# Kernel tuning notes

Hardware: AMD Instinct MI355X
Metric: run time of the kernel (lower is better)

Reference implementation:

```python
import jax, jax.numpy as jnp
from jax import lax
import numpy as np

K = 8          # local window radius -> (2K+1)^2 = 289 offsets
TOPK = 256     # topk channels kept for fg/bg correlation
EPS = 1e-5     # torch InstanceNorm2d default eps


def _conv3(x, w, b):
    # 3x3 conv, stride 1, pad 1, NCHW/OIHW
    y = lax.conv_general_dilated(x, w, (1, 1), ((1, 1), (1, 1)),
                                 dimension_numbers=('NCHW', 'OIHW', 'NCHW'))
    return y + b[None, :, None, None]


def _inorm(x):
    # InstanceNorm2d(affine=False): per (b,c) normalization over HxW, biased var
    m = jnp.mean(x, axis=(2, 3), keepdims=True)
    v = jnp.mean((x - m) ** 2, axis=(2, 3), keepdims=True)
    return (x - m) * lax.rsqrt(v + EPS)


def _aic(x, w1, b1, w2, b2):
    # AIC(in, hidden): conv3x3(in->hidden)+IN+ReLU -> conv3x3(hidden->in)+IN+ReLU
    h = jax.nn.relu(_inorm(_conv3(x, w1, b1)))
    return jax.nn.relu(_inorm(_conv3(h, w2, b2)))


def _amaxpool(x, H, W):
    # adaptive_max_pool2d with exact integer factor (384/48 = 8)
    kh, kw = x.shape[2] // H, x.shape[3] // W
    return lax.reduce_window(x, -jnp.inf, lax.max, (1, 1, kh, kw), (1, 1, kh, kw), 'VALID')


def _topk_c(x, k=TOPK):
    # topk over channel axis, values sorted descending (matches torch.topk)
    v, _ = lax.top_k(jnp.transpose(x, (0, 2, 3, 1)), k)  # [B,H,W,k]
    return jnp.transpose(v, (0, 3, 1, 2))                 # [B,k,H,W]


def _resize_ac(x, H, W):
    # bilinear interpolate, align_corners=True
    B, C, h, w = x.shape
    def grid(n_out, n_in):
        if n_out == 1:
            return jnp.zeros((1,), jnp.float32)
        return jnp.arange(n_out, dtype=jnp.float32) * ((n_in - 1) / (n_out - 1))
    ys, xs = grid(H, h), grid(W, w)
    y0 = jnp.clip(jnp.floor(ys).astype(jnp.int32), 0, h - 1)
    y1 = jnp.minimum(y0 + 1, h - 1)
    x0 = jnp.clip(jnp.floor(xs).astype(jnp.int32), 0, w - 1)
    x1 = jnp.minimum(x0 + 1, w - 1)
    wy = (ys - y0.astype(jnp.float32))[None, None, :, None]
    wx = (xs - x0.astype(jnp.float32))[None, None, None, :]
    rows = x[:, :, y0, :] * (1.0 - wy) + x[:, :, y1, :] * wy  # [B,C,H,w]
    return rows[:, :, :, x0] * (1.0 - wx) + rows[:, :, :, x1] * wx


def _forward(p3, p2, p1, kg1, klp, key_mask, pre_mask,
             conv_top_w, conv_top_b,
             aic_top_w1, aic_top_b1, aic_top_w2, aic_top_b2,
             r1a_w1, r1a_b1, r1a_w2, r1a_b2,
             r1b_w1, r1b_b1, r1b_w2, r1b_b2,
             r2a_w1, r2a_b1, r2a_w2, r2a_b2,
             r2b_w1, r2b_b1, r2b_w2, r2b_b2,
             dec_conv1_w, dec_conv1_b, pred_w, pred_b):
    B, _, H, W = kg1.shape  # kg1: [B, H*W, H, W]
    # --- Global, mode=2: fg/bg topk over the global correlation volume ---
    gm = _amaxpool(key_mask, H, W).reshape(B, H * W, 1, 1)
    gf = _topk_c(kg1 * gm)
    gb = _topk_c(kg1 * (1.0 - gm))
    # --- Local, mode=2: unfold mask into 17x17 windows, fg/bg topk ---
    lm = _amaxpool(pre_mask, H, W)                       # [B,1,H,W]
    lmp = jnp.pad(lm, ((0, 0), (0, 0), (K, K), (K, K)))  # zero pad (FF.pad default)
    patches = lax.conv_general_dilated_patches(
        lmp, (2 * K + 1, 2 * K + 1), (1, 1), 'VALID',
        dimension_numbers=('NCHW', 'OIHW', 'NCHW'))      # [B,289,H,W], ch = dy*17+dx
    lf = _topk_c(klp * patches)
    lb = _topk_c(klp * (1.0 - patches))
    # --- fuse at p3 resolution ---
    pm = _amaxpool(pre_mask, H, W)
    x = jnp.concatenate([p3, gf, gb, lf, lb, pm], axis=1)  # [B, 256*5+1, H, W]
    x = _conv3(x, conv_top_w, conv_top_b)                  # 1281 -> 256
    x = _aic(x, aic_top_w1, aic_top_b1, aic_top_w2, aic_top_b2)
    # --- Decoder: Refine(256,64) -> conv 256->64 -> Refine(64,64) -> pred ---
    y = _resize_ac(x, p2.shape[2], p2.shape[3])
    y = _aic(y, r1a_w1, r1a_b1, r1a_w2, r1a_b2)
    y = y + p2
    y = _aic(y, r1b_w1, r1b_b1, r1b_w2, r1b_b2)
    y = _conv3(y, dec_conv1_w, dec_conv1_b)
    z = _resize_ac(y, p1.shape[2], p1.shape[3])
    z = _aic(z, r2a_w1, r2a_b1, r2a_w2, r2a_b2)
    z = z + p1
    z = _aic(z, r2b_w1, r2b_b1, r2b_w2, r2b_b2)
    return jax.nn.sigmoid(_conv3(z, pred_w, pred_b))       # [B,1,192,192]


def setup_inputs() -> dict:
    key = jax.random.key(0)
    ks = jax.random.split(key, 40)
    B, H, W = 2, 48, 48
    inp = {}
    inp['p3'] = jax.random.normal(ks[0], (B, 256, H, W), jnp.float32)
    inp['p2'] = jax.random.normal(ks[1], (B, 256, 2 * H, 2 * W), jnp.float32)
    inp['p1'] = jax.random.normal(ks[2], (B, 64, 4 * H, 4 * W), jnp.float32)
    inp['kg1'] = jax.random.normal(ks[3], (B, H * W, H, W), jnp.float32)
    inp['klp'] = jax.random.normal(ks[4], (B, (2 * K + 1) ** 2, H, W), jnp.float32)
    inp['key_mask'] = jax.random.uniform(ks[5], (B, 1, 8 * H, 8 * W), dtype=jnp.float32)
    inp['pre_mask'] = jax.random.uniform(ks[6], (B, 1, 8 * H, 8 * W), dtype=jnp.float32)
    i = [7]
    def p(shape, s=0.05):
        w = jax.random.normal(ks[i[0]], shape, jnp.float32) * s
        i[0] += 1
        return w
    inp['conv_top_w'] = p((256, 256 * 5 + 1, 3, 3))
    inp['conv_top_b'] = jnp.zeros((256,), jnp.float32)
    for nm, (ci, ch) in [('aic_top', (256, 64)), ('r1a', (256, 64)), ('r1b', (256, 64)),
                         ('r2a', (64, 64)), ('r2b', (64, 64))]:
        inp[nm + '_w1'] = p((ch, ci, 3, 3)); inp[nm + '_b1'] = jnp.zeros((ch,), jnp.float32)
        inp[nm + '_w2'] = p((ci, ch, 3, 3)); inp[nm + '_b2'] = jnp.zeros((ci,), jnp.float32)
    inp['dec_conv1_w'] = p((64, 256, 3, 3)); inp['dec_conv1_b'] = jnp.zeros((64,), jnp.float32)
    inp['pred_w'] = p((1, 64, 3, 3)); inp['pred_b'] = jnp.zeros((1,), jnp.float32)
    return inp


def reference(p3, p2, p1, kg1, klp, key_mask, pre_mask,
              conv_top_w, conv_top_b,
              aic_top_w1, aic_top_b1, aic_top_w2, aic_top_b2,
              r1a_w1, r1a_b1, r1a_w2, r1a_b2,
              r1b_w1, r1b_b1, r1b_w2, r1b_b2,
              r2a_w1, r2a_b1, r2a_w2, r2a_b2,
              r2b_w1, r2b_b1, r2b_w2, r2b_b2,
              dec_conv1_w, dec_conv1_b, pred_w, pred_b):
    return _forward(p3, p2, p1, kg1, klp, key_mask, pre_mask,
                    conv_top_w, conv_top_b,
                    aic_top_w1, aic_top_b1, aic_top_w2, aic_top_b2,
                    r1a_w1, r1a_b1, r1a_w2, r1a_b2,
                    r1b_w1, r1b_b1, r1b_w2, r1b_b2,
                    r2a_w1, r2a_b1, r2a_w2, r2a_b2,
                    r2b_w1, r2b_b1, r2b_w2, r2b_b2,
                    dec_conv1_w, dec_conv1_b, pred_w, pred_b)
```

## Files before the change

### kernel.cpp

```cpp
#include <hip/hip_runtime.h>
#include <math.h>

#define TPB 256

typedef _Float16 h8 __attribute__((ext_vector_type(8)));
typedef float f4 __attribute__((ext_vector_type(4)));
typedef unsigned short ushort_t;

__device__ __forceinline__ unsigned short f2bf(float x) {
  unsigned int u = __float_as_uint(x);
  unsigned int r = (u + 0x7fffu + ((u >> 16) & 1u)) >> 16;
  return (unsigned short)r;
}
__device__ __forceinline__ float bf2f(unsigned short h) {
  return __uint_as_float(((unsigned int)h) << 16);
}
__device__ __forceinline__ ushort_t f2h(float x) {
  _Float16 h = (_Float16)x;
  return *(ushort_t*)&h;
}
__device__ __forceinline__ float h2f(ushort_t u) {
  _Float16 h = *(_Float16*)&u;
  return (float)h;
}
__device__ __forceinline__ unsigned key16_of(float x) {
  unsigned h = (unsigned)f2h(x);
  return h ^ ((h >> 15) ? 0xFFFFu : 0x8000u);
}
__device__ __forceinline__ ushort_t un_key16(unsigned k) {
  return (ushort_t)(k ^ ((k & 0x8000u) ? 0x8000u : 0xFFFFu));
}

__global__ __launch_bounds__(TPB) void pool8_kernel(const float* __restrict__ in,
                                                    float* __restrict__ out, int total) {
  int idx = blockIdx.x * TPB + threadIdx.x;
  if (idx >= total) return;
  int b = idx / 2304, yx = idx - b * 2304;
  int y = yx / 48, x = yx - y * 48;
  const float* p = in + ((size_t)b * 384 + (size_t)y * 8) * 384 + (size_t)x * 8;
  float m = -INFINITY;
#pragma unroll
  for (int i = 0; i < 8; ++i)
#pragma unroll
    for (int j = 0; j < 8; ++j) m = fmaxf(m, p[(size_t)i * 384 + j]);
  out[idx] = m;
}

__global__ __launch_bounds__(TPB) void tposef_kernel(const float* __restrict__ src,
                                                     float* __restrict__ dst, int C, int HW,
                                                     int DS) {
  __shared__ float tile[64][65];
  int px0 = blockIdx.x * 64;
  int c0 = blockIdx.y * 64;
  int b = blockIdx.z;
  int tid = threadIdx.x;
#pragma unroll
  for (int i = 0; i < 16; ++i) {
    int c = (tid >> 6) + i * 4, p = tid & 63;
    tile[c][p] = src[((size_t)b * C + c0 + c) * HW + px0 + p];
  }
  __syncthreads();
#pragma unroll
  for (int i = 0; i < 16; ++i) {
    int c = tid & 63, p = (tid >> 6) + i * 4;
    dst[((size_t)b * HW + px0 + p) * DS + c0 + c] = tile[c][p];
  }
}

__global__ __launch_bounds__(TPB) void tposeg_kernel(const float* __restrict__ src,
                                                     float* __restrict__ dst, int C, int HW,
                                                     int DS) {
  __shared__ float tile[64][65];
  int px0 = blockIdx.x * 64;
  int c0 = blockIdx.y * 64;
  int b = blockIdx.z;
  int tid = threadIdx.x;
#pragma unroll
  for (int i = 0; i < 16; ++i) {
    int c = (tid >> 6) + i * 4, p = tid & 63;
    float v = 0.f;
    if (c0 + c < C) v = src[((size_t)b * C + c0 + c) * HW + px0 + p];
    tile[c][p] = v;
  }
  __syncthreads();
#pragma unroll
  for (int i = 0; i < 16; ++i) {
    int c = tid & 63, p = (tid >> 6) + i * 4;
    if (c0 + c < C)
      dst[((size_t)b * HW + px0 + p) * DS + c0 + c] = tile[c][p];
  }
}

__global__ __launch_bounds__(TPB) void tposeh_kernel(const float* __restrict__ src,
                                                     ushort_t* __restrict__ dst, int C, int HW,
                                                     int DS) {
  __shared__ float tile[64][65];
  int px0 = blockIdx.x * 64;
  int c0 = blockIdx.y * 64;
  int b = blockIdx.z;
  int tid = threadIdx.x;
#pragma unroll
  for (int i = 0; i < 16; ++i) {
    int c = (tid >> 6) + i * 4, p = tid & 63;
    tile[c][p] = src[((size_t)b * C + c0 + c) * HW + px0 + p];
  }
  __syncthreads();
#pragma unroll
  for (int i = 0; i < 16; ++i) {
    int c = tid & 63, p = (tid >> 6) + i * 4;
    dst[((size_t)b * HW + px0 + p) * DS + c0 + c] = f2h(tile[c][p]);
  }
}

__global__ __launch_bounds__(TPB) void topk_global_kernel(const float* __restrict__ kgT,
                                                          const float* __restrict__ gm,
                                                          ushort_t* __restrict__ xcat) {
  __shared__ unsigned histF[4][256], histB[4][256];
  __shared__ ushort_t soutF[256], soutB[256];
  __shared__ unsigned selT[2], selA[2];
  __shared__ unsigned cntG[2], cntE[2];
  const int tid = threadIdx.x;
  const int lane = tid & 63, wid = tid >> 6;
  int bid = blockIdx.x;
  int b = bid / 2304, yx = bid - b * 2304;
  const float* kp = kgT + ((size_t)b * 2304 + yx) * 2304;
  const float* gp = gm + (size_t)b * 2304;
  unsigned kF[9], kB[9];
#pragma unroll
  for (int j = 0; j < 9; ++j) {
    int i = tid + 256 * j;
    float v = kp[i];
    float g = gp[i];
    kF[j] = key16_of(v * g);
    kB[j] = key16_of(v * (1.0f - g));
  }
#pragma unroll
  for (int w = 0; w < 4; ++w) {
    histF[w][tid] = 0;
    histB[w][tid] = 0;
  }
  __syncthreads();
#pragma unroll
  for (int j = 0; j < 9; ++j) {
    atomicAdd(&histF[wid][kF[j] >> 8], 1u);
    atomicAdd(&histB[wid][kB[j] >> 8], 1u);
  }
  __syncthreads();
  if (wid < 2) {
    unsigned(*hh)[256] = wid ? histB : histF;
    unsigned h0 = hh[0][4 * lane] + hh[1][4 * lane] + hh[2][4 * lane] + hh[3][4 * lane];
    unsigned h1 = hh[0][4 * lane + 1] + hh[1][4 * lane + 1] + hh[2][4 * lane + 1] +
                  hh[3][4 * lane + 1];
    unsigned h2 = hh[0][4 * lane + 2] + hh[1][4 * lane + 2] + hh[2][4 * lane + 2] +
                  hh[3][4 * lane + 2];
    unsigned h3 = hh[0][4 * lane + 3] + hh[1][4 * lane + 3] + hh[2][4 * lane + 3] +
                  hh[3][4 * lane + 3];
    unsigned x = h0 + h1 + h2 + h3;
#pragma unroll
    for (int d = 1; d < 64; d <<= 1) {
      unsigned y = __shfl_down(x, d, 64);
      if (lane + d < 64) x += y;
    }
    unsigned long long m = __ballot(x >= 256u);
    int tl = 63 - __clzll(m);
    if (lane == tl) {
      unsigned s1 = x - h0, s2 = s1 - h1, s3 = s2 - h2, s4 = s3 - h3;
      int jj;
      unsigned A;
      if (s3 >= 256u) { jj = 3; A = s4; }
      else if (s2 >= 256u) { jj = 2; A = s3; }
      else if (s1 >= 256u) { jj = 1; A = s2; }
      else { jj = 0; A = s1; }
      selT[wid] = 4 * tl + jj;
      selA[wid] = A;
    }
  }
  __syncthreads();
  const unsigned T0F = selT[0], gt0F = selA[0];
  const unsigned T0B = selT[1], gt0B = selA[1];
  const unsigned KF = 256u - gt0F, KB = 256u - gt0B;
  histF[0][tid] = 0;
  histB[0][tid] = 0;
  __syncthreads();
#pragma unroll
  for (int j = 0; j < 9; ++j) {
    if ((kF[j] >> 8) == T0F) atomicAdd(&histF[0][kF[j] & 0xFFu], 1u);
    if ((kB[j] >> 8) == T0B) atomicAdd(&histB[0][kB[j] & 0xFFu], 1u);
  }
  __syncthreads();
  if (wid < 2) {
    unsigned* h = wid ? histB[0] : histF[0];
    unsigned K = wid ? KB : KF;
    unsigned h0 = h[4 * lane], h1 = h[4 * lane + 1];
    unsigned h2 = h[4 * lane + 2], h3 = h[4 * lane + 3];
    unsigned x = h0 + h1 + h2 + h3;
#pragma unroll
    for (int d = 1; d < 64; d <<= 1) {
      unsigned y = __shfl_down(x, d, 64);
      if (lane + d < 64) x += y;
    }
    unsigned long long m = __ballot(x >= K);
    int tl = 63 - __clzll(m);
    if (lane == tl) {
      unsigned s1 = x - h0, s2 = s1 - h1, s3 = s2 - h2, s4 = s3 - h3;
      int jj;
      unsigned A;
      if (s3 >= K) { jj = 3; A = s4; }
      else if (s2 >= K) { jj = 2; A = s3; }
      else if (s1 >= K) { jj = 1; A = s2; }
      else { jj = 0; A = s1; }
      selT[wid] = 4 * tl + jj;
      selA[wid] = A;
    }
  }
  __syncthreads();
  const unsigned tF = (T0F << 8) | selT[0];
  const unsigned tB = (T0B << 8) | selT[1];
  const unsigned nGTF = gt0F + selA[0], needF = 256u - nGTF;
  const unsigned nGTB = gt0B + selA[1], needB = 256u - nGTB;
  if (tid == 0) { cntG[0] = 0; cntG[1] = 0; cntE[0] = 0; cntE[1] = 0; }
  __syncthreads();
#pragma unroll
  for (int j = 0; j < 9; ++j) {
    unsigned k = kF[j];
    if (k > tF) soutF[atomicAdd(&cntG[0], 1u)] = (ushort_t)k;
    else if (k == tF) {
      unsigned e = atomicAdd(&cntE[0], 1u);
      if (e < needF) soutF[nGTF + e] = (ushort_t)tF;
    }
    k = kB[j];
    if (k > tB) soutB[atomicAdd(&cntG[1], 1u)] = (ushort_t)k;
    else if (k == tB) {
      unsigned e = atomicAdd(&cntE[1], 1u);
      if (e < needB) soutB[nGTB + e] = (ushort_t)tB;
    }
  }
  __syncthreads();
  if (wid < 2) {
    ushort_t* sarr = wid ? soutB : soutF;
    for (int kk = 2; kk <= 256; kk <<= 1) {
      for (int j = kk >> 1; j > 0; j >>= 1) {
#pragma unroll
        for (int r = 0; r < 2; ++r) {
          int p = lane + r * 64;
          int t = (p & (j - 1)) | ((p & ~(j - 1)) << 1);
          int ixj = t | j;
          bool up = ((t & kk) == 0);
          ushort_t a = sarr[t], c = sarr[ixj];
          if (up ? (a > c) : (a < c)) { sarr[t] = c; sarr[ixj] = a; }
        }
        __builtin_amdgcn_wave_barrier();
      }
    }
  }
  __syncthreads();
  size_t base = ((size_t)(b * 2304 + yx)) * 1312;
  xcat[base + 256 + tid] = un_key16((unsigned)soutF[255 - tid]);
  xcat[base + 512 + tid] = un_key16((unsigned)soutB[255 - tid]);
}

__global__ __launch_bounds__(64) void topk_local_kernel(const float* __restrict__ klpT,
                                                        const float* __restrict__ lm,
                                                        ushort_t* __restrict__ xcat) {
  __shared__ float sf[512];
  __shared__ float sb[512];
  const int lane = threadIdx.x;
  const int pix = blockIdx.x;
  const int b = pix / 2304;
  const int yx = pix - b * 2304;
  const int y = yx / 48, x = yx - y * 48;
  const float* kp = klpT + (size_t)pix * 320;
#pragma unroll
  for (int r = 0; r < 8; ++r) {
    int i = lane + r * 64;
    float vf = -INFINITY, vb = -INFINITY;
    if (i < 289) {
      int dy = i / 17, dx = i - dy * 17;
      int sy = y + dy - 8, sx = x + dx - 8;
      float pv = 0.f;
      if (sy >= 0 && sy < 48 && sx >= 0 && sx < 48) pv = lm[(size_t)b * 2304 + sy * 48 + sx];
      float v = kp[i];
      vf = v * pv;
      vb = v * (1.0f - pv);
    }
    sf[i] = vf;
    sb[i] = vb;
  }
  __builtin_amdgcn_wave_barrier();
  for (int k = 2; k <= 512; k <<= 1) {
    for (int j = k >> 1; j > 0; j >>= 1) {
#pragma unroll
      for (int r = 0; r < 4; ++r) {
        int p = lane + r * 64;
        int t = (p & (j - 1)) | ((p & ~(j - 1)) << 1);
        int ixj = t | j;
        bool up = ((t & k) == 0);
        float a = sf[t], c = sf[ixj];
        if (up ? (a > c) : (a < c)) { sf[t] = c; sf[ixj] = a; }
        a = sb[t]; c = sb[ixj];
        if (up ? (a > c) : (a < c)) { sb[t] = c; sb[ixj] = a; }
      }
      __builtin_amdgcn_wave_barrier();
    }
  }
  size_t base = (size_t)pix * 1312;
#pragma unroll
  for (int r = 0; r < 4; ++r) {
    int t = lane + r * 64;
    xcat[base + 768 + t] = f2h(sf[511 - t]);
    xcat[base + 1024 + t] = f2h(sb[511 - t]);
  }
}

__global__ __launch_bounds__(TPB) void pm_pad_kernel(const float* __restrict__ lm,
                                                     ushort_t* __restrict__ xcat) {
  int idx = blockIdx.x * TPB + threadIdx.x;
  if (idx >= 2 * 2304 * 32) return;
  int ch = idx & 31;
  int r = idx >> 5;
  xcat[(size_t)r * 1312 + 1280 + ch] = (ch == 0) ? f2h(lm[r]) : (ushort_t)0;
}

struct WallDesc {
  const float* src[13];
  int CinW[13], CIP[13], CoutPad[13], CoutReal[13];
  unsigned start[14];
  int n;
};
__global__ __launch_bounds__(TPB) void wconv_all_kernel(WallDesc D, ushort_t* __restrict__ whi,
                                                        int total) {
  int i = blockIdx.x * TPB + threadIdx.x;
  if (i >= total) return;
  int k = 0;
  while (k + 1 < D.n && (unsigned)i >= D.start[k + 1]) ++k;
  int j = i - D.start[k];
  int e = j & 7;
  int t = j >> 3;
  int l16 = t & 15; t >>= 4;
  int h4 = t & 3; t >>= 2;
  int NCOG = D.CoutPad[k] >> 4;
  int cog = t % NCOG; t /= NCOG;
  int kykx = t % 9;
  int chunk = t / 9;
  int co = cog * 16 + l16;
  int ci = chunk * 32 + h4 * 8 + e;
  float v = 0.f;
  if (ci < D.CinW[k] && co < D.CoutReal[k])
    v = D.src[k][((size_t)co * D.CinW[k] + ci) * 9 + kykx];
  whi[i] = f2h(v);
}

template <int NORM>
__device__ __forceinline__ uint4 norm8(uint4 v, const float* __restrict__ nmean,
                                       const float* __restrict__ ninv,
                                       const void* __restrict__ nres, size_t mb,
                                       size_t pxoff) {
  float f[8];
  f[0] = h2f((ushort_t)(v.x & 0xffff)); f[1] = h2f((ushort_t)(v.x >> 16));
  f[2] = h2f((ushort_t)(v.y & 0xffff)); f[3] = h2f((ushort_t)(v.y >> 16));
  f[4] = h2f((ushort_t)(v.z & 0xffff)); f[5] = h2f((ushort_t)(v.z >> 16));
  f[6] = h2f((ushort_t)(v.w & 0xffff)); f[7] = h2f((ushort_t)(v.w >> 16));
  float4 m0 = *(const float4*)(nmean + mb);
  float4 m1 = *(const float4*)(nmean + mb + 4);
  float4 i0 = *(const float4*)(ninv + mb);
  float4 i1 = *(const float4*)(ninv + mb + 4);
  float o[8];
  o[0] = fmaxf((f[0] - m0.x) * i0.x, 0.f);
  o[1] = fmaxf((f[1] - m0.y) * i0.y, 0.f);
  o[2] = fmaxf((f[2] - m0.z) * i0.z, 0.f);
  o[3] = fmaxf((f[3] - m0.w) * i0.w, 0.f);
  o[4] = fmaxf((f[4] - m1.x) * i1.x, 0.f);
  o[5] = fmaxf((f[5] - m1.y) * i1.y, 0.f);
  o[6] = fmaxf((f[6] - m1.z) * i1.z, 0.f);
  o[7] = fmaxf((f[7] - m1.w) * i1.w, 0.f);
  if (NORM == 2) {
    uint4 rv = *(const uint4*)((const ushort_t*)nres + pxoff);
    o[0] += h2f((ushort_t)(rv.x & 0xffff)); o[1] += h2f((ushort_t)(rv.x >> 16));
    o[2] += h2f((ushort_t)(rv.y & 0xffff)); o[3] += h2f((ushort_t)(rv.y >> 16));
    o[4] += h2f((ushort_t)(rv.z & 0xffff)); o[5] += h2f((ushort_t)(rv.z >> 16));
    o[6] += h2f((ushort_t)(rv.w & 0xffff)); o[7] += h2f((ushort_t)(rv.w >> 16));
  } else if (NORM == 3) {
    const float* rp = (const float*)nres + pxoff;
    float4 r0 = *(const float4*)rp;
    float4 r1 = *(const float4*)(rp + 4);
    o[0] += r0.x; o[1] += r0.y; o[2] += r0.z; o[3] += r0.w;
    o[4] += r1.x; o[5] += r1.y; o[6] += r1.z; o[7] += r1.w;
  }
  uint4 out;
  out.x = (unsigned)f2h(o[0]) | ((unsigned)f2h(o[1]) << 16);
  out.y = (unsigned)f2h(o[2]) | ((unsigned)f2h(o[3]) << 16);
  out.z = (unsigned)f2h(o[4]) | ((unsigned)f2h(o[5]) << 16);
  out.w = (unsigned)f2h(o[6]) | ((unsigned)f2h(o[7]) << 16);
  return out;
}

template <int MFR, int ACT, int STAT, int GEOM, int NORM>
__global__ __launch_bounds__(TPB) void conv_mfma_kernel(
    const ushort_t* __restrict__ in, const ushort_t* __restrict__ whi,
    const float* __restrict__ bias,
    ushort_t* __restrict__ outh, float* __restrict__ outf, ushort_t* __restrict__ partial,
    float* __restrict__ stat, int ntiles,
    const float* __restrict__ nmean, const float* __restrict__ ninv,
    const void* __restrict__ nres,
    int hin, int win, float rs,
    int CIP, int Cout, int H, int W, int S, int ci_per_s) {
  const int NPIX = (GEOM == 1) ? 100 : 180;
  const int PITCH = 10;
  __shared__ uint4 sB[(GEOM == 1) ? 800 : 1440];
  const int MB = (GEOM == 1) ? 64 : MFR * 32;
  const int tid = threadIdx.x;
  const int lane = tid & 63;
  const int lo16 = lane & 15, hi4 = lane >> 4;
  const int wid = tid >> 6;
  const int wco = (GEOM == 1) ? wid : (wid & 1);
  const int wpx = (GEOM == 1) ? 0 : (wid >> 1);
  const int tilesX = W >> 3;
  const int tx0 = (blockIdx.x % tilesX) << 3;
  const int ty0 = (blockIdx.x / tilesX) << ((GEOM == 1) ? 3 : 4);
  const int s = blockIdx.y % S;
  const int co0 = (blockIdx.y / S) * MB;
  const int b = blockIdx.z;
  const int NCOG = Cout >> 4;
  const size_t HW = (size_t)H * W;
  const ushort_t* inb = in + (size_t)b * HW * CIP;
  const ushort_t* srcb = in + (size_t)b * hin * win * CIP;
  int ci_begin = s * ci_per_s;
  int ci_end = ci_begin + ci_per_s;
  if (ci_end > CIP) ci_end = CIP;
  f4 acc[MFR][4];
#pragma unroll
  for (int m = 0; m < MFR; ++m)
#pragma unroll
    for (int n = 0; n < 4; ++n) acc[m][n] = (f4){0.f, 0.f, 0.f, 0.f};

  for (int ci0 = ci_begin; ci0 < ci_end; ci0 += 64) {
    const bool has2 = (ci0 + 32 < ci_end);
    __syncthreads();
#pragma unroll
    for (int it = 0; it < 6; ++it) {
      int u = it * TPB + tid;
      if (u < NPIX * 8) {
        int q4 = u / NPIX;
        int pix = u - q4 * NPIX;
        int prow = pix / PITCH, pcol = pix - prow * PITCH;
        int gy = ty0 - 1 + prow, gx = tx0 - 1 + pcol;
        int ci = ci0 + q4 * 8;
        bool inbp = (ci < CIP && gy >= 0 && gy < H && gx >= 0 && gx < W);
        uint4 v = {0u, 0u, 0u, 0u};
        if (inbp) {
          if (NORM <= 3) {
            v = *(const uint4*)(inb + ((size_t)gy * W + gx) * CIP + ci);
            if (NORM != 0) {
              size_t mb = (size_t)b * CIP + ci;
              size_t pxoff = ((size_t)b * HW + (size_t)gy * W + gx) * CIP + ci;
              v = norm8<NORM>(v, nmean, ninv, nres, mb, pxoff);
            }
          } else {
            float ys = gy * rs, xs = gx * rs;
            int y0 = (int)floorf(ys);
            if (y0 > hin - 1) y0 = hin - 1;
            int x0 = (int)floorf(xs);
            if (x0 > win - 1) x0 = win - 1;
            int y1 = y0 + 1 < hin ? y0 + 1 : hin - 1;
            int x1 = x0 + 1 < win ? x0 + 1 : win - 1;
            float wy = ys - (float)y0, wx = xs - (float)x0;
            uint4 s00 = *(const uint4*)(srcb + ((size_t)y0 * win + x0) * CIP + ci);
            uint4 s01 = *(const uint4*)(srcb + ((size_t)y0 * win + x1) * CIP + ci);
            uint4 s10 = *(const uint4*)(srcb + ((size_t)y1 * win + x0) * CIP + ci);
            uint4 s11 = *(const uint4*)(srcb + ((size_t)y1 * win + x1) * CIP + ci);
            float w00 = (1.f - wy) * (1.f - wx), w01 = (1.f - wy) * wx;
            float w10 = wy * (1.f - wx), w11 = wy * wx;
            union U8 { uint4 q; ushort_t sv[8]; };
            U8 u00, u01, u10, u11, uo;
            u00.q = s00; u01.q = s01; u10.q = s10; u11.q = s11;
#pragma unroll
            for (int k8 = 0; k8 < 8; ++k8) {
              float val = h2f(u00.sv[k8]) * w00 + h2f(u01.sv[k8]) * w01 +
                          h2f(u10.sv[k8]) * w10 + h2f(u11.sv[k8]) * w11;
              uo.sv[k8] = f2h(val);
            }
            v = uo.q;
          }
        }
        sB[q4 * NPIX + pix] = v;
      }
    }
    __syncthreads();
#pragma unroll
    for (int h = 0; h < 2; ++h) {
      if (h == 1 && !has2) continue;
      const int chunkIdx = (ci0 >> 5) + h;
#pragma unroll
      for (int ky = 0; ky < 3; ++ky) {
#pragma unroll
        for (int kx = 0; kx < 3; ++kx) {
          const int kykx = ky * 3 + kx;
          h8 ah[MFR];
#pragma unroll
          for (int m = 0; m < MFR; ++m) {
            int cog = (co0 + wco * (GEOM == 1 ? 16 : (MB / 2)) + m * 16) >> 4;
            size_t woff = (((size_t)chunkIdx * 9 + kykx) * NCOG + cog) * 512 + (size_t)lane * 8;
            ah[m] = *(const h8*)(whi + woff);
          }
          h8 bf[4];
#pragma unroll
          for (int n = 0; n < 4; ++n) {
            int pix = (wpx * 8 + n * 2 + (lo16 >> 3) + ky) * PITCH + (lo16 & 7) + kx;
            union { uint4 q; h8 v; } ub;
            ub.q = sB[(h * 4 + hi4) * NPIX + pix];
            bf[n] = ub.v;
          }
#pragma unroll
          for (int m = 0; m < MFR; ++m)
#pragma unroll
            for (int n = 0; n < 4; ++n)
              acc[m][n] = __builtin_amdgcn_mfma_f32_16x16x32_f16(ah[m], bf[n], acc[m][n], 0, 0, 0);
        }
      }
    }
  }

#pragma unroll
  for (int m = 0; m < MFR; ++m) {
#pragma unroll
    for (int n = 0; n < 4; ++n) {
      int py = ty0 + wpx * 8 + n * 2 + (lo16 >> 3);
      int pxx = tx0 + (lo16 & 7);
      int co_r0 = co0 + wco * (GEOM == 1 ? 16 : (MB / 2)) + m * 16 + hi4 * 4;
      if (ACT == 1) {
        if (wco == 0 && m == 0 && hi4 == 0) {
          float v = acc[0][n][0] + bias[0];
          outf[(size_t)b * HW + (size_t)py * W + pxx] = 1.0f / (1.0f + expf(-v));
        }
      } else if (S == 1) {
        float4 bv = *(const float4*)(bias + co_r0);
        unsigned w0 = (unsigned)f2h(acc[m][n][0] + bv.x) |
                      ((unsigned)f2h(acc[m][n][1] + bv.y) << 16);
        unsigned w1 = (unsigned)f2h(acc[m][n][2] + bv.z) |
                      ((unsigned)f2h(acc[m][n][3] + bv.w) << 16);
        uint2 o = {w0, w1};
        *(uint2*)(outh + (((size_t)b * HW + (size_t)py * W + pxx) * Cout + co_r0)) = o;
        if (STAT) {
          acc[m][n][0] = h2f((ushort_t)(w0 & 0xffff));
          acc[m][n][1] = h2f((ushort_t)(w0 >> 16));
          acc[m][n][2] = h2f((ushort_t)(w1 & 0xffff));
          acc[m][n][3] = h2f((ushort_t)(w1 >> 16));
        }
      } else {
        uint2 o;
        o.x = (unsigned)f2h(acc[m][n][0]) | ((unsigned)f2h(acc[m][n][1]) << 16);
        o.y = (unsigned)f2h(acc[m][n][2]) | ((unsigned)f2h(acc[m][n][3]) << 16);
        *(uint2*)(partial + (((size_t)(s * 2 + b) * HW + (size_t)py * W + pxx) * Cout + co_r0)) = o;
      }
    }
  }

  if (STAT) {
    __syncthreads();
    f4* lredS = (f4*)sB;
    f4* lredQ = lredS + 32;
    if (GEOM == 1) {
      f4 sv = acc[0][0] + acc[0][1] + acc[0][2] + acc[0][3];
      f4 qv = acc[0][0] * acc[0][0] + acc[0][1] * acc[0][1] + acc[0][2] * acc[0][2] +
              acc[0][3] * acc[0][3];
#pragma unroll
      for (int off = 1; off < 16; off <<= 1) {
#pragma unroll
        for (int kq = 0; kq < 4; ++kq) {
          sv[kq] += __shfl_xor(sv[kq], off, 64);
          qv[kq] += __shfl_xor(qv[kq], off, 64);
        }
      }
      if (lo16 == 0) {
        lredS[wid * 4 + hi4] = sv;
        lredQ[wid * 4 + hi4] = qv;
      }
      __syncthreads();
      if (tid < 16) {
        int widT = tid >> 2, h4T = tid & 3;
        int c = co0 + widT * 16 + h4T * 4;
        size_t sbase = ((size_t)b * ntiles + blockIdx.x) * (size_t)(Cout * 2);
        *(f4*)(stat + sbase + c) = lredS[tid];
        *(f4*)(stat + sbase + Cout + c) = lredQ[tid];
      }
    } else {
#pragma unroll
      for (int m = 0; m < MFR; ++m) {
        f4 sv = acc[m][0] + acc[m][1] + acc[m][2] + acc[m][3];
        f4 qv = acc[m][0] * acc[m][0] + acc[m][1] * acc[m][1] + acc[m][2] * acc[m][2] +
                acc[m][3] * acc[m][3];
#pragma unroll
        for (int off = 1; off < 16; off <<= 1) {
#pragma unroll
          for (int kq = 0; kq < 4; ++kq) {
            sv[kq] += __shfl_xor(sv[kq], off, 64);
            qv[kq] += __shfl_xor(qv[kq], off, 64);
          }
        }
        if (lo16 == 0) {
          lredS[(wid * MFR + m) * 4 + hi4] = sv;
          lredQ[(wid * MFR + m) * 4 + hi4] = qv;
        }
      }
      __syncthreads();
      if (tid < 2 * MFR * 4) {
        int wcoT = tid / (MFR * 4);
        int r = tid % (MFR * 4);
        int mT = r / 4;
        int h4T = r % 4;
        f4 sv = lredS[((wcoT)*MFR + mT) * 4 + h4T] + lredS[((wcoT + 2) * MFR + mT) * 4 + h4T];
        f4 qv = lredQ[((wcoT)*MFR + mT) * 4 + h4T] + lredQ[((wcoT + 2) * MFR + mT) * 4 + h4T];
        int c = co0 + wcoT * (MB / 2) + mT * 16 + h4T * 4;
        size_t sbase = ((size_t)b * ntiles + blockIdx.x) * (size_t)(Cout * 2);
        *(f4*)(stat + sbase + c) = sv;
        *(f4*)(stat + sbase + Cout + c) = qv;
      }
    }
  }
}

__global__ __launch_bounds__(TPB) void pred_kernel(const ushort_t* __restrict__ in,
                                                   const float* __restrict__ w,
                                                   const float* __restrict__ bias,
                                                   const float* __restrict__ nmean,
                                                   const float* __restrict__ ninv,
                                                   float* __restrict__ outp) {
  __shared__ uint4 hal[324 * 9];
  __shared__ float wl[576];
  const int tid = threadIdx.x;
  const int tx0 = (blockIdx.x % 12) * 16;
  const int ty0 = (blockIdx.x / 12) * 16;
  const int b = blockIdx.y;
  const ushort_t* inb = in + (size_t)b * 36864 * 64;
  for (int u = tid; u < 576; u += TPB) {
    int ci = u & 63, kk = u >> 6;
    wl[u] = w[(size_t)ci * 9 + kk];
  }
  for (int u = tid; u < 2592; u += TPB) {
    int px = u >> 3, q4 = u & 7;
    int r = px / 18, c = px - r * 18;
    int gy = ty0 - 1 + r, gx = tx0 - 1 + c;
    uint4 v = {0u, 0u, 0u, 0u};
    if (gy >= 0 && gy < 192 && gx >= 0 && gx < 192) {
      v = *(const uint4*)(inb + ((size_t)gy * 192 + gx) * 64 + q4 * 8);
      v = norm8<1>(v, nmean, ninv, nullptr, (size_t)b * 64 + q4 * 8, 0);
    }
    hal[px * 9 + q4] = v;
  }
  __syncthreads();
  const int ty = tid >> 4, tx = tid & 15;
  float acc = bias[0];
#pragma unroll
  for (int ky = 0; ky < 3; ++ky) {
#pragma unroll
    for (int kx = 0; kx < 3; ++kx) {
      int base = ((ty + ky) * 18 + tx + kx) * 9;
      const float* wp = &wl[(ky * 3 + kx) * 64];
#pragma unroll
      for (int q = 0; q < 8; ++q) {
        uint4 v = hal[base + q];
        const float* w8 = wp + q * 8;
        acc = fmaf(h2f((ushort_t)(v.x & 0xffff)), w8[0], acc);
        acc = fmaf(h2f((ushort_t)(v.x >> 16)), w8[1], acc);
        acc = fmaf(h2f((ushort_t)(v.y & 0xffff)), w8[2], acc);
        acc = fmaf(h2f((ushort_t)(v.y >> 16)), w8[3], acc);
        acc = fmaf(h2f((ushort_t)(v.z & 0xffff)), w8[4], acc);
        acc = fmaf(h2f((ushort_t)(v.z >> 16)), w8[5], acc);
        acc = fmaf(h2f((ushort_t)(v.w & 0xffff)), w8[6], acc);
        acc = fmaf(h2f((ushort_t)(v.w >> 16)), w8[7], acc);
      }
    }
  }
  outp[(size_t)b * 36864 + (size_t)(ty0 + ty) * 192 + (tx0 + tx)] =
      1.0f / (1.0f + expf(-acc));
}

template <int STAT>
__global__ __launch_bounds__(TPB) void reduce_nhwc_kernel(const ushort_t* __restrict__ partial,
                                                          const float* __restrict__ bias,
                                                          ushort_t* __restrict__ outh,
                                                          float* __restrict__ stat, int bpb,
                                                          int S, int Cout, int HW, int total4) {
  int i = blockIdx.x * TPB + threadIdx.x;
  float4 accv = {0.f, 0.f, 0.f, 0.f};
  unsigned w0 = 0, w1 = 0;
  int e = i * 4;
  int CHW = Cout * HW;
  if (i < total4) {
    int b = e / CHW;
    int rem = e - b * CHW;
    int co = e % Cout;
    for (int ss = 0; ss < S; ++ss) {
      const uint2 t2 = *(const uint2*)(partial + (size_t)(ss * 2 + b) * CHW + rem);
      accv.x += h2f((ushort_t)(t2.x & 0xffff));
      accv.y += h2f((ushort_t)(t2.x >> 16));
      accv.z += h2f((ushort_t)(t2.y & 0xffff));
      accv.w += h2f((ushort_t)(t2.y >> 16));
    }
    float4 bv = *(const float4*)(bias + co);
    w0 = (unsigned)f2h(accv.x + bv.x) | ((unsigned)f2h(accv.y + bv.y) << 16);
    w1 = (unsigned)f2h(accv.z + bv.z) | ((unsigned)f2h(accv.w + bv.w) << 16);
    uint2 o = {w0, w1};
    *(uint2*)(outh + (size_t)b * CHW + rem) = o;
  }
  if (STAT) {
    __shared__ f4 ls[4][16], lq[4][16];
    const int tid = threadIdx.x;
    const int lane = tid & 63, wv = tid >> 6;
    f4 r;
    r[0] = h2f((ushort_t)(w0 & 0xffff));
    r[1] = h2f((ushort_t)(w0 >> 16));
    r[2] = h2f((ushort_t)(w1 & 0xffff));
    r[3] = h2f((ushort_t)(w1 >> 16));
    f4 sv = r;
    f4 qv = r * r;
#pragma unroll
    for (int kq = 0; kq < 4; ++kq) {
      sv[kq] += __shfl_down(sv[kq], 16, 64);
      qv[kq] += __shfl_down(qv[kq], 16, 64);
      sv[kq] += __shfl_down(sv[kq], 32, 64);
      qv[kq] += __shfl_down(qv[kq], 32, 64);
    }
    if (lane < 16) {
      ls[wv][lane] = sv;
      lq[wv][lane] = qv;
    }
    __syncthreads();
    if (tid < 16) {
      f4 S4 = ls[0][tid] + ls[1][tid] + ls[2][tid] + ls[3][tid];
      f4 Q4 = lq[0][tid] + lq[1][tid] + lq[2][tid] + lq[3][tid];
      int b = (blockIdx.x * (TPB * 4)) / CHW;
      int tblk = blockIdx.x - b * bpb;
      int c = tid * 4;
      size_t sbase = ((size_t)b * bpb + tblk) * (size_t)(Cout * 2);
      *(f4*)(stat + sbase + c) = S4;
      *(f4*)(stat + sbase + Cout + c) = Q4;
    }
  }
}

__global__ __launch_bounds__(TPB) void in_stats_kernel(const ushort_t* __restrict__ x,
                                                       float* __restrict__ stat, int N, int C) {
  __shared__ float ls[4][64], lq[4][64];
  int CG = C >> 6;
  int b = blockIdx.x / CG, cg = blockIdx.x % CG;
  int slice = blockIdx.y;
  int c = threadIdx.x & 63, p = threadIdx.x >> 6;
  int cnt = N >> 6;
  int base = slice * cnt;
  float s = 0.f, q = 0.f;
  const ushort_t* xp = x + ((size_t)b * N) * C + cg * 64 + c;
  for (int px = base + p; px < base + cnt; px += 4) {
    float v = h2f(xp[(size_t)px * C]);
    s += v;
    q = fmaf(v, v, q);
  }
  ls[p][c] = s;
  lq[p][c] = q;
  __syncthreads();
  if (threadIdx.x < 64) {
    float S = ls[0][threadIdx.x] + ls[1][threadIdx.x] + ls[2][threadIdx.x] + ls[3][threadIdx.x];
    float Q = lq[0][threadIdx.x] + lq[1][threadIdx.x] + lq[2][threadIdx.x] + lq[3][threadIdx.x];
    int Ctot = 2 * C;
    int idx = b * C + cg * 64 + threadIdx.x;
    stat[(size_t)(slice * Ctot + idx) * 2] = S;
    stat[(size_t)(slice * Ctot + idx) * 2 + 1] = Q;
  }
}

__global__ __launch_bounds__(TPB) void in_final_kernel(const float* __restrict__ stat,
                                                       float* __restrict__ mean,
                                                       float* __restrict__ inv, int N, int Ctot) {
  int idx = blockIdx.x * TPB + threadIdx.x;
  if (idx >= Ctot) return;
  float S = 0.f, Q = 0.f;
  for (int sl = 0; sl < 64; ++sl) {
    S += stat[(size_t)(sl * Ctot + idx) * 2];
    Q += stat[(size_t)(sl * Ctot + idx) * 2 + 1];
  }
  float m = S / (float)N;
  float var = Q / (float)N - m * m;
  if (var < 0.f) var = 0.f;
  mean[idx] = m;
  inv[idx] = 1.0f / sqrtf(var + 1e-5f);
}

__global__ __launch_bounds__(TPB) void in_final_tiles_kernel(const float* __restrict__ stat,
                                                             float* __restrict__ mean,
                                                             float* __restrict__ inv, int N,
                                                             int C, int ntiles) {
  __shared__ float rs_[TPB], rq_[TPB];
  int idx = blockIdx.x;
  int b = idx / C, c = idx % C;
  float S = 0.f, Q = 0.f;
  for (int t = threadIdx.x; t < ntiles; t += TPB) {
    size_t base = ((size_t)b * ntiles + t) * (size_t)(C * 2);
    S += stat[base + c];
    Q += stat[base + C + c];
  }
  rs_[threadIdx.x] = S;
  rq_[threadIdx.x] = Q;
  __syncthreads();
  for (int off = TPB / 2; off > 0; off >>= 1) {
    if (threadIdx.x < off) {
      rs_[threadIdx.x] += rs_[threadIdx.x + off];
      rq_[threadIdx.x] += rq_[threadIdx.x + off];
    }
    __syncthreads();
  }
  if (threadIdx.x == 0) {
    float ma = rs_[0] / (float)N;
    float var = rq_[0] / (float)N - ma * ma;
    if (var < 0.f) var = 0.f;
    mean[idx] = ma;
    inv[idx] = 1.0f / sqrtf(var + 1e-5f);
  }
}

template <int NORM>
__global__ __launch_bounds__(TPB) void resize4_kernel(const ushort_t* __restrict__ in,
                                                      ushort_t* __restrict__ out,
                                                      const float* __restrict__ nmean,
                                                      const float* __restrict__ ninv, int C,
                                                      int hin, int win, int Hout, int Wout,
                                                      float r, int total4) {
  for (int i = blockIdx.x * TPB + threadIdx.x; i < total4; i += gridDim.x * TPB) {
    int e = i * 4;
    int c = e % C;
    int t = e / C;
    int X = t % Wout;
    int t2 = t / Wout;
    int Y = t2 % Hout;
    int b = t2 / Hout;
    float ys = Y * r, xs = X * r;
    int y0 = (int)floorf(ys);
    if (y0 > hin - 1) y0 = hin - 1;
    int x0 = (int)floorf(xs);
    if (x0 > win - 1) x0 = win - 1;
    int y1 = y0 + 1 < hin ? y0 + 1 : hin - 1;
    int x1 = x0 + 1 < win ? x0 + 1 : win - 1;
    float wy = ys - (float)y0, wx = xs - (float)x0;
    const ushort_t* ip = in + ((size_t)b * hin * win) * C + c;
    uint2 a2 = *(const uint2*)(ip + ((size_t)y0 * win + x0) * C);
    uint2 b2 = *(const uint2*)(ip + ((size_t)y0 * win + x1) * C);
    uint2 c2 = *(const uint2*)(ip + ((size_t)y1 * win + x0) * C);
    uint2 d2 = *(const uint2*)(ip + ((size_t)y1 * win + x1) * C);
    float av[4], bv[4], cv[4], dv[4];
    av[0] = h2f((ushort_t)(a2.x & 0xffff)); av[1] = h2f((ushort_t)(a2.x >> 16));
    av[2] = h2f((ushort_t)(a2.y & 0xffff)); av[3] = h2f((ushort_t)(a2.y >> 16));
    bv[0] = h2f((ushort_t)(b2.x & 0xffff)); bv[1] = h2f((ushort_t)(b2.x >> 16));
    bv[2] = h2f((ushort_t)(b2.y & 0xffff)); bv[3] = h2f((ushort_t)(b2.y >> 16));
    cv[0] = h2f((ushort_t)(c2.x & 0xffff)); cv[1] = h2f((ushort_t)(c2.x >> 16));
    cv[2] = h2f((ushort_t)(c2.y & 0xffff)); cv[3] = h2f((ushort_t)(c2.y >> 16));
    dv[0] = h2f((ushort_t)(d2.x & 0xffff)); dv[1] = h2f((ushort_t)(d2.x >> 16));
    dv[2] = h2f((ushort_t)(d2.y & 0xffff)); dv[3] = h2f((ushort_t)(d2.y >> 16));
    if (NORM) {
      float4 m4 = *(const float4*)(nmean + (size_t)b * C + c);
      float4 i4 = *(const float4*)(ninv + (size_t)b * C + c);
      float mm[4] = {m4.x, m4.y, m4.z, m4.w};
      float ii[4] = {i4.x, i4.y, i4.z, i4.w};
#pragma unroll
      for (int k = 0; k < 4; ++k) {
        av[k] = fmaxf((av[k] - mm[k]) * ii[k], 0.f);
        bv[k] = fmaxf((bv[k] - mm[k]) * ii[k], 0.f);
        cv[k] = fmaxf((cv[k] - mm[k]) * ii[k], 0.f);
        dv[k] = fmaxf((dv[k] - mm[k]) * ii[k], 0.f);
      }
    }
    float w00 = (1.f - wy) * (1.f - wx), w01 = (1.f - wy) * wx;
    float w10 = wy * (1.f - wx), w11 = wy * wx;
    float o[4];
#pragma unroll
    for (int k = 0; k < 4; ++k)
      o[k] = av[k] * w00 + bv[k] * w01 + cv[k] * w10 + dv[k] * w11;
    uint2 ov;
    ov.x = (unsigned)f2h(o[0]) | ((unsigned)f2h(o[1]) << 16);
    ov.y = (unsigned)f2h(o[2]) | ((unsigned)f2h(o[3]) << 16);
    *(uint2*)(out + e) = ov;
  }
}

extern "C" void kernel_launch(void* const* d_in, const int* in_sizes, int n_in,
                              void* d_out, int out_size, void* d_ws, size_t ws_size,
                              hipStream_t stream) {
  (void)in_sizes; (void)n_in; (void)out_size;
  const float* p3 = (const float*)d_in[0];
  const float* p2 = (const float*)d_in[1];
  const float* p1 = (const float*)d_in[2];
  const float* kg1 = (const float*)d_in[3];
  const float* klp = (const float*)d_in[4];
  const float* key_mask = (const float*)d_in[5];
  const float* pre_mask = (const float*)d_in[6];
  const float* conv_top_w = (const float*)d_in[7];
  const float* conv_top_b = (const float*)d_in[8];
  const float* aic_top_w1 = (const float*)d_in[9];
  const float* aic_top_b1 = (const float*)d_in[10];
  const float* aic_top_w2 = (const float*)d_in[11];
  const float* aic_top_b2 = (const float*)d_in[12];
  const float* r1a_w1 = (const float*)d_in[13];
  const float* r1a_b1 = (const float*)d_in[14];
  const float* r1a_w2 = (const float*)d_in[15];
  const float* r1a_b2 = (const float*)d_in[16];
  const float* r1b_w1 = (const float*)d_in[17];
  const float* r1b_b1 = (const float*)d_in[18];
  const float* r1b_w2 = (const float*)d_in[19];
  const float* r1b_b2 = (const float*)d_in[20];
  const float* r2a_w1 = (const float*)d_in[21];
  const float* r2a_b1 = (const float*)d_in[22];
  const float* r2a_w2 = (const float*)d_in[23];
  const float* r2a_b2 = (const float*)d_in[24];
  const float* r2b_w1 = (const float*)d_in[25];
  const float* r2b_b1 = (const float*)d_in[26];
  const float* r2b_w2 = (const float*)d_in[27];
  const float* r2b_b2 = (const float*)d_in[28];
  const float* dec_w = (const float*)d_in[29];
  const float* dec_b = (const float*)d_in[30];
  const float* pred_w = (const float*)d_in[31];
  const float* pred_b = (const float*)d_in[32];
  float* outp = (float*)d_out;

  const size_t OFF_GM = 0;
  const size_t OFF_LM = 4608;
  const size_t OFF_STAT = 9216;
  const size_t OFF_MEAN = 304128;
  const size_t OFF_INV = 304640;
  const size_t OFF_WB = 305152;
  const size_t OFF_AH0 = 4544512;
  const size_t OFF_AH1 = 7567360;
  const size_t OFF_AH2 = 8157184;
  const size_t OFF_AH3 = 8304640;
  const size_t OFF_AH4 = 8894464;
  const size_t OFF_AH5 = 11253760;
  const size_t OFF_P1T = 13613056;
  const size_t OFF_P2T = 18331648;
  const size_t TOTAL_F = 19511296;
  if (ws_size < TOTAL_F * sizeof(float)) return;

  float* ws = (float*)d_ws;
  float* gm = ws + OFF_GM;
  float* lm = ws + OFF_LM;
  float* statb = ws + OFF_STAT;
  float* meanb = ws + OFF_MEAN;
  float* invb = ws + OFF_INV;
  ushort_t* wbh = (ushort_t*)(ws + OFF_WB);
  ushort_t* xcat_h = (ushort_t*)(ws + OFF_AH0);
  ushort_t* y96_h = (ushort_t*)(ws + OFF_AH0);
  ushort_t* a0_h = (ushort_t*)(ws + OFF_AH1);
  ushort_t* h96_h = (ushort_t*)(ws + OFF_AH1);
  ushort_t* d96_h = (ushort_t*)(ws + OFF_AH1);
  ushort_t* h48_h = (ushort_t*)(ws + OFF_AH2);
  ushort_t* a1_h = (ushort_t*)(ws + OFF_AH3);
  ushort_t* R1_h = (ushort_t*)(ws + OFF_AH4);
  ushort_t* zA_h = (ushort_t*)(ws + OFF_AH4);
  ushort_t* R0_h = (ushort_t*)(ws + OFF_AH5);
  ushort_t* zB_h = (ushort_t*)(ws + OFF_AH5);
  ushort_t* Pbuf16 = (ushort_t*)(ws + OFF_P1T);
  ushort_t* PbufTop16 = (ushort_t*)(ws + OFF_AH4);
  float* p1t = ws + OFF_P1T;
  ushort_t* p2t = (ushort_t*)(ws + OFF_P2T);
  float* kgT = ws + OFF_AH4;
  float* klpT = ws + OFF_P1T;

  WallDesc D;
  const float* wsrc[13] = {conv_top_w, aic_top_w1, aic_top_w2, r1a_w1, r1a_w2, r1b_w1,
                           r1b_w2, dec_w, r2a_w1, r2a_w2, r2b_w1, r2b_w2, pred_w};
  const int wcin[13] = {1281, 256, 64, 256, 64, 256, 64, 256, 64, 64, 64, 64, 64};
  const int wcip[13] = {1312, 256, 64, 256, 64, 256, 64, 256, 64, 64, 64, 64, 64};
  const int wcop[13] = {256, 64, 256, 64, 256, 64, 256, 64, 64, 64, 64, 64, 64};
  const int wcor[13] = {256, 64, 256, 64, 256, 64, 256, 64, 64, 64, 64, 64, 1};
  unsigned cum = 0;
  unsigned woff[13];
  for (int k = 0; k < 13; ++k) {
    D.src[k] = wsrc[k];
    D.CinW[k] = wcin[k];
    D.CIP[k] = wcip[k];
    D.CoutPad[k] = wcop[k];
    D.CoutReal[k] = wcor[k];
    D.start[k] = cum;
    woff[k] = cum;
    cum += (unsigned)(wcop[k] * 9 * wcip[k]);
  }
  D.start[13] = cum;
  D.n = 13;
  wconv_all_kernel<<<(cum + TPB - 1) / TPB, TPB, 0, stream>>>(D, wbh, (int)cum);

  pool8_kernel<<<(2 * 2304 + TPB - 1) / TPB, TPB, 0, stream>>>(key_mask, gm, 2 * 2304);
  pool8_kernel<<<(2 * 2304 + TPB - 1) / TPB, TPB, 0, stream>>>(pre_mask, lm, 2 * 2304);
  tposeg_kernel<<<dim3(36, 5, 2), TPB, 0, stream>>>(klp, klpT, 289, 2304, 320);
  topk_local_kernel<<<4608, 64, 0, stream>>>(klpT, lm, xcat_h);
  tposef_kernel<<<dim3(36, 36, 2), TPB, 0, stream>>>(kg1, kgT, 2304, 2304, 2304);
  topk_global_kernel<<<2 * 2304, TPB, 0, stream>>>(kgT, gm, xcat_h);
  tposeh_kernel<<<dim3(36, 4, 2), TPB, 0, stream>>>(p3, xcat_h, 256, 2304, 1312);
  pm_pad_kernel<<<(2 * 2304 * 32 + TPB - 1) / TPB, TPB, 0, stream>>>(lm, xcat_h);

  auto conv = [&](const ushort_t* src, int wk, const float* bb, ushort_t* dsth,
                  ushort_t* part, int CIP, int CoutPad, int H, int W, int S, int MB,
                  int geom, int redStat, int normMode, const void* res, int hin, int win,
                  float rsc) {
    const ushort_t* whiK = wbh + woff[wk];
    int chunks = CIP / 32;
    int cps = ((chunks + S - 1) / S) * 32;
    if (geom == 1) {
      int ntiles = (W / 8) * (H / 8);
      dim3 grid(ntiles, CoutPad / 64, 2);
      if (normMode == 1)
        conv_mfma_kernel<1, 0, 1, 1, 1><<<grid, TPB, 0, stream>>>(
            src, whiK, bb, dsth, nullptr, nullptr, statb, ntiles, meanb, invb, res,
            hin, win, rsc, CIP, CoutPad, H, W, 1, cps);
      else if (normMode == 3)
        conv_mfma_kernel<1, 0, 1, 1, 3><<<grid, TPB, 0, stream>>>(
            src, whiK, bb, dsth, nullptr, nullptr, statb, ntiles, meanb, invb, res,
            hin, win, rsc, CIP, CoutPad, H, W, 1, cps);
      else if (normMode == 5)
        conv_mfma_kernel<1, 0, 1, 1, 5><<<grid, TPB, 0, stream>>>(
            src, whiK, bb, dsth, nullptr, nullptr, statb, ntiles, meanb, invb, res,
            hin, win, rsc, CIP, CoutPad, H, W, 1, cps);
      else
        conv_mfma_kernel<1, 0, 1, 1, 0><<<grid, TPB, 0, stream>>>(
            src, whiK, bb, dsth, nullptr, nullptr, statb, ntiles, meanb, invb, res,
            hin, win, rsc, CIP, CoutPad, H, W, 1, cps);
      return;
    }
    int ntiles = (W / 8) * (H / 16);
    dim3 grid(ntiles, (CoutPad / MB) * S, 2);
    if (MB == 128)
      conv_mfma_kernel<4, 0, 0, 0, 0><<<grid, TPB, 0, stream>>>(
          src, whiK, bb, dsth, nullptr, part, nullptr, 0, meanb, invb, res, hin, win,
          rsc, CIP, CoutPad, H, W, S, cps);
    else if (normMode == 1)
      conv_mfma_kernel<2, 0, 0, 0, 1><<<grid, TPB, 0, stream>>>(
          src, whiK, bb, dsth, nullptr, part, nullptr, 0, meanb, invb, res, hin, win,
          rsc, CIP, CoutPad, H, W, S, cps);
    else if (normMode == 2)
      conv_mfma_kernel<2, 0, 0, 0, 2><<<grid, TPB, 0, stream>>>(
          src, whiK, bb, dsth, nullptr, part, nullptr, 0, meanb, invb, res, hin, win,
          rsc, CIP, CoutPad, H, W, S, cps);
    else
      conv_mfma_kernel<2, 0, 0, 0, 0><<<grid, TPB, 0, stream>>>(
          src, whiK, bb, dsth, nullptr, part, nullptr, 0, meanb, invb, res, hin, win,
          rsc, CIP, CoutPad, H, W, S, cps);
    if (S > 1) {
      int HW = H * W;
      int total4 = 2 * CoutPad * HW / 4;
      int nblk = (total4 + TPB - 1) / TPB;
      int bpb = (CoutPad * HW) / (TPB * 4);
      if (redStat)
        reduce_nhwc_kernel<1><<<nblk, TPB, 0, stream>>>(part, bb, dsth, statb, bpb, S,
                                                        CoutPad, HW, total4);
      else
        reduce_nhwc_kernel<0><<<nblk, TPB, 0, stream>>>(part, bb, dsth, nullptr, 0, S,
                                                        CoutPad, HW, total4);
    }
  };
  auto stats_plain = [&](ushort_t* x, int C, int N) {
    dim3 g1(2 * (C / 64), 64);
    in_stats_kernel<<<g1, TPB, 0, stream>>>(x, statb, N, C);
    int Ctot = 2 * C;
    in_final_kernel<<<(Ctot + TPB - 1) / TPB, TPB, 0, stream>>>(statb, meanb, invb, N, Ctot);
  };
  auto stats_tiles = [&](int C, int N, int ntiles) {
    in_final_tiles_kernel<<<2 * C, TPB, 0, stream>>>(statb, meanb, invb, N, C, ntiles);
  };

  conv(xcat_h, 0, conv_top_b, a0_h, PbufTop16, 1312, 256, 48, 48, 7, 128, 0, 0, 0, nullptr,
       48, 48, 1.f);
  conv(a0_h, 1, aic_top_b1, h48_h, Pbuf16, 256, 64, 48, 48, 8, 64, 0, 1, 0, nullptr, 48, 48,
       1.f);
  stats_tiles(64, 2304, 144);
  conv(h48_h, 2, aic_top_b2, a1_h, Pbuf16, 64, 256, 48, 48, 2, 64, 0, 0, 1, nullptr, 48, 48,
       1.f);
  stats_plain(a1_h, 256, 2304);

  {
    int total4 = 2 * 96 * 96 * 256 / 4;
    int g = (total4 + TPB - 1) / TPB; if (g > 4096) g = 4096;
    resize4_kernel<1><<<g, TPB, 0, stream>>>(a1_h, y96_h, meanb, invb, 256, 48, 48, 96, 96,
                                             47.f / 95.f, total4);
  }
  conv(y96_h, 3, r1a_b1, h96_h, Pbuf16, 256, 64, 96, 96, 4, 64, 0, 1, 0, nullptr, 96, 96,
       1.f);
  tposeh_kernel<<<dim3(144, 4, 2), TPB, 0, stream>>>(p2, p2t, 256, 9216, 256);
  stats_tiles(64, 9216, 576);
  conv(h96_h, 4, r1a_b2, R1_h, nullptr, 64, 256, 96, 96, 1, 64, 1, 0, 1, nullptr, 96, 96,
       1.f);
  stats_tiles(256, 9216, 144);
  conv(R1_h, 5, r1b_b1, h96_h, Pbuf16, 256, 64, 96, 96, 4, 64, 0, 1, 2, p2t, 96, 96, 1.f);
  stats_tiles(64, 9216, 576);
  conv(h96_h, 6, r1b_b2, R0_h, nullptr, 64, 256, 96, 96, 1, 64, 1, 0, 1, nullptr, 96, 96,
       1.f);
  stats_tiles(256, 9216, 144);
  conv(R0_h, 7, dec_b, d96_h, Pbuf16, 256, 64, 96, 96, 4, 64, 0, 0, 1, nullptr, 96, 96,
       1.f);
  tposef_kernel<<<dim3(576, 1, 2), TPB, 0, stream>>>(p1, p1t, 64, 36864, 64);

  conv(d96_h, 8, r2a_b1, zA_h, nullptr, 64, 64, 192, 192, 1, 64, 1, 0, 5, nullptr, 96, 96,
       95.f / 191.f);
  stats_tiles(64, 36864, 576);
  conv(zA_h, 9, r2a_b2, zB_h, nullptr, 64, 64, 192, 192, 1, 64, 1, 0, 1, nullptr, 192, 192,
       1.f);
  stats_tiles(64, 36864, 576);
  conv(zB_h, 10, r2b_b1, zA_h, nullptr, 64, 64, 192, 192, 1, 64, 1, 0, 3, p1t, 192, 192,
       1.f);
  stats_tiles(64, 36864, 576);
  conv(zA_h, 11, r2b_b2, zB_h, nullptr, 64, 64, 192, 192, 1, 64, 1, 0, 1, nullptr, 192, 192,
       1.f);
  stats_tiles(64, 36864, 576);

  pred_kernel<<<dim3(144, 2), TPB, 0, stream>>>(zB_h, pred_w, pred_b, meanb, invb, outp);
}
```

Before: 517.6 us.

## Run local top-k bitonic sort in registers with wave shuffles

The local-window top-k bitonic sort now keeps its 512 values in per-lane registers (8 per lane) instead of LDS. Compare-exchange steps with stride of 64 or more happen between registers inside a lane, and smaller strides use cross-lane xor shuffles. Four pixels are packed into each 256-thread block instead of one 64-thread block per pixel. This removes LDS traffic and wave barriers from a small kernel, at the cost of more shuffle instructions and register use.

New measurement: 514.3 us. No clear change (-0.6%).

```diff
diff --git a/kernel.cpp b/kernel.cpp
--- a/kernel.cpp
+++ b/kernel.cpp
@@ -259,20 +259,20 @@
   xcat[base + 512 + tid] = un_key16((unsigned)soutB[255 - tid]);
 }
 
-__global__ __launch_bounds__(64) void topk_local_kernel(const float* __restrict__ klpT,
-                                                        const float* __restrict__ lm,
-                                                        ushort_t* __restrict__ xcat) {
-  __shared__ float sf[512];
-  __shared__ float sb[512];
-  const int lane = threadIdx.x;
-  const int pix = blockIdx.x;
+__global__ __launch_bounds__(TPB) void topk_local_kernel(const float* __restrict__ klpT,
+                                                         const float* __restrict__ lm,
+                                                         ushort_t* __restrict__ xcat) {
+  const int lane = threadIdx.x & 63;
+  const int wid = threadIdx.x >> 6;
+  const int pix = blockIdx.x * 4 + wid;
   const int b = pix / 2304;
   const int yx = pix - b * 2304;
   const int y = yx / 48, x = yx - y * 48;
   const float* kp = klpT + (size_t)pix * 320;
+  float vF[8], vB[8];
 #pragma unroll
   for (int r = 0; r < 8; ++r) {
-    int i = lane + r * 64;
+    int i = r * 64 + lane;
     float vf = -INFINITY, vb = -INFINITY;
     if (i < 289) {
       int dy = i / 17, dx = i - dy * 17;
@@ -283,32 +283,49 @@
       vf = v * pv;
       vb = v * (1.0f - pv);
     }
-    sf[i] = vf;
-    sb[i] = vb;
-  }
-  __builtin_amdgcn_wave_barrier();
+    vF[r] = vf;
+    vB[r] = vb;
+  }
   for (int k = 2; k <= 512; k <<= 1) {
     for (int j = k >> 1; j > 0; j >>= 1) {
-#pragma unroll
-      for (int r = 0; r < 4; ++r) {
-        int p = lane + r * 64;
-        int t = (p & (j - 1)) | ((p & ~(j - 1)) << 1);
-        int ixj = t | j;
-        bool up = ((t & k) == 0);
-        float a = sf[t], c = sf[ixj];
-        if (up ? (a > c) : (a < c)) { sf[t] = c; sf[ixj] = a; }
-        a = sb[t]; c = sb[ixj];
-        if (up ? (a > c) : (a < c)) { sb[t] = c; sb[ixj] = a; }
+      if (j >= 64) {
+        const int jr = j >> 6;
+#pragma unroll
+        for (int r = 0; r < 8; ++r) {
+          if ((r & jr) == 0) {
+            const int rp = r | jr;
+            bool up = (((unsigned)(r * 64) & (unsigned)k) == 0);
+            float aF = vF[r], cF = vF[rp];
+            float aB = vB[r], cB = vB[rp];
+            if (up) {
+              vF[r] = fminf(aF, cF); vF[rp] = fmaxf(aF, cF);
+              vB[r] = fminf(aB, cB); vB[rp] = fmaxf(aB, cB);
+            } else {
+              vF[r] = fmaxf(aF, cF); vF[rp] = fminf(aF, cF);
+              vB[r] = fmaxf(aB, cB); vB[rp] = fminf(aB, cB);
+            }
+          }
+        }
+      } else {
+        bool lower = ((lane & j) == 0);
+#pragma unroll
+        for (int r = 0; r < 8; ++r) {
+          float pF = __shfl_xor(vF[r], j, 64);
+          float pB = __shfl_xor(vB[r], j, 64);
+          bool up = (((unsigned)(r * 64 + lane) & (unsigned)k) == 0);
+          bool takeMin = (lower == up);
+          vF[r] = takeMin ? fminf(vF[r], pF) : fmaxf(vF[r], pF);
+          vB[r] = takeMin ? fminf(vB[r], pB) : fmaxf(vB[r], pB);
+        }
       }
-      __builtin_amdgcn_wave_barrier();
     }
   }
   size_t base = (size_t)pix * 1312;
 #pragma unroll
-  for (int r = 0; r < 4; ++r) {
-    int t = lane + r * 64;
-    xcat[base + 768 + t] = f2h(sf[511 - t]);
-    xcat[base + 1024 + t] = f2h(sb[511 - t]);
+  for (int r = 4; r < 8; ++r) {
+    int t = 511 - (r * 64 + lane);
+    xcat[base + 768 + t] = f2h(vF[r]);
+    xcat[base + 1024 + t] = f2h(vB[r]);
   }
 }
 
@@ -987,7 +1004,7 @@
   pool8_kernel<<<(2 * 2304 + TPB - 1) / TPB, TPB, 0, stream>>>(key_mask, gm, 2 * 2304);
   pool8_kernel<<<(2 * 2304 + TPB - 1) / TPB, TPB, 0, stream>>>(pre_mask, lm, 2 * 2304);
   tposeg_kernel<<<dim3(36, 5, 2), TPB, 0, stream>>>(klp, klpT, 289, 2304, 320);
-  topk_local_kernel<<<4608, 64, 0, stream>>>(klpT, lm, xcat_h);
+  topk_local_kernel<<<1152, TPB, 0, stream>>>(klpT, lm, xcat_h);
   tposef_kernel<<<dim3(36, 36, 2), TPB, 0, stream>>>(kg1, kgT, 2304, 2304, 2304);
   topk_global_kernel<<<2 * 2304, TPB, 0, stream>>>(kgT, gm, xcat_h);
   tposeh_kernel<<<dim3(36, 4, 2), TPB, 0, stream>>>(p3, xcat_h, 256, 2304, 1312);
```
